# Kernel tuning notes

Measured on AMD Instinct MI355X. Metric: run time of the kernel, lower is better.

Reference implementation:

```python
import jax, jax.numpy as jnp
import numpy as np

NUM_TREES = 32
NUM_NODES = 6
SEED = 0
BATCH, CH, T = 16, 128, 4096


def _make_forest(num_trees, num_nodes, seed):
    """Random rooted trees: node 0 is root, node i>0 attaches to a uniform
    random earlier node (classic random recursive tree). Returns, per tree,
    the children-list representation."""
    rng = np.random.default_rng(seed)
    forest = []
    for _ in range(num_trees):
        children = [[] for _ in range(num_nodes)]
        for i in range(1, num_nodes):
            p = int(rng.integers(0, i))
            children[p].append(i)
        forest.append(children)
    return forest


def _excl_cumsum(u):
    # sum_{s < t} u[..., s]  (exclusive prefix sum along the ordered axis)
    return jnp.cumsum(u, axis=-1) - u


def _sum_trees(x, alphas, forest):
    """Iterated-sums evaluation over a forest in the (plus, times) semiring.
    Node value: v_i(t) = alpha_i * x(t) * prod_{c in children(i)} sum_{s<t} v_c(s).
    Tree output: sum_t v_root(t), per channel. x: [B,C,T]. Returns [B,num_trees,C]."""
    outs = []
    for t_idx, children in enumerate(forest):
        vals = {}
        for i in reversed(range(len(children))):  # leaves-to-root order
            v = alphas[t_idx, i][None, :, None] * x  # [B,C,T]
            for c in children[i]:
                v = v * _excl_cumsum(vals.pop(c))
            vals[i] = v
        outs.append(jnp.sum(vals[0], axis=-1))  # [B,C]
    return jnp.stack(outs, axis=1)  # [B,num_trees,C]


def setup_inputs() -> dict:
    key = jax.random.key(0)
    k1, k2 = jax.random.split(key)
    x = jax.random.normal(k1, (BATCH, CH, T), dtype=jnp.float32)
    alphas = jax.random.normal(k2, (NUM_TREES, NUM_NODES, CH), dtype=jnp.float32)
    return {"x": x, "alphas": alphas}


def reference(x, alphas):
    forest = _make_forest(NUM_TREES, NUM_NODES, SEED)
    return _sum_trees(x, alphas, forest)
```

## Files before the change

kernel.cpp:

```cpp
#include <hip/hip_runtime.h>
#include <cstdint>
#include <cstddef>

namespace cx {

constexpr uint32_t hashmix(uint32_t value, uint32_t& hc) {
    value ^= hc; hc *= 0x931e8875u; value *= hc; value ^= value >> 16; return value;
}
constexpr uint32_t mixf(uint32_t x, uint32_t y) {
    uint32_t r = x * 0xca01f9ddu - y * 0x4973f715u; r ^= r >> 16; return r;
}

struct Pcg64 {
    unsigned __int128 state{}, inc{};
    bool has_uint32{}; uint32_t uinteger{};
    static constexpr unsigned __int128 mult() {
        return (((unsigned __int128)2549297995355413924ULL) << 64) | 4865540595714422341ULL;
    }
    constexpr void step() { state = state * mult() + inc; }
    constexpr void seed_default0() {
        uint32_t pool[4] = {0, 0, 0, 0};
        uint32_t hc = 0x43b0d7e5u;
        for (int i = 0; i < 4; ++i) pool[i] = hashmix(0u, hc);
        for (int isrc = 0; isrc < 4; ++isrc)
            for (int idst = 0; idst < 4; ++idst)
                if (isrc != idst) pool[idst] = mixf(pool[idst], hashmix(pool[isrc], hc));
        uint32_t st[8] = {};
        uint32_t hc2 = 0x8b51f9ddu;
        for (int i = 0; i < 8; ++i) {
            uint32_t dv = pool[i & 3];
            dv ^= hc2; hc2 *= 0x58f38dedu; dv *= hc2; dv ^= dv >> 16;
            st[i] = dv;
        }
        const uint64_t v0 = (uint64_t)st[0] | ((uint64_t)st[1] << 32);
        const uint64_t v1 = (uint64_t)st[2] | ((uint64_t)st[3] << 32);
        const uint64_t v2 = (uint64_t)st[4] | ((uint64_t)st[5] << 32);
        const uint64_t v3 = (uint64_t)st[6] | ((uint64_t)st[7] << 32);
        const unsigned __int128 s = (((unsigned __int128)v0) << 64) | v1;
        const unsigned __int128 i_ = (((unsigned __int128)v2) << 64) | v3;
        state = 0; inc = (i_ << 1) | 1;
        step(); state += s; step();
        has_uint32 = false; uinteger = 0;
    }
    constexpr uint64_t next64() {
        step();
        const uint64_t hi = (uint64_t)(state >> 64), lo = (uint64_t)state;
        const uint64_t x = hi ^ lo;
        const unsigned rot = (unsigned)(state >> 122);
        return (x >> rot) | (x << ((64u - rot) & 63u));
    }
    constexpr uint32_t next32() {
        if (has_uint32) { has_uint32 = false; return uinteger; }
        const uint64_t n = next64();
        has_uint32 = true; uinteger = (uint32_t)(n >> 32);
        return (uint32_t)n;
    }
    constexpr uint32_t bounded_lemire32(uint32_t rng) {
        const uint32_t rng_excl = rng + 1u;
        uint64_t m = (uint64_t)next32() * (uint64_t)rng_excl;
        uint32_t leftover = (uint32_t)m;
        if (leftover < rng_excl) {
            const uint32_t threshold = (0xFFFFFFFFu - rng) % rng_excl;
            while (leftover < threshold) {
                m = (uint64_t)next32() * (uint64_t)rng_excl;
                leftover = (uint32_t)m;
            }
        }
        return (uint32_t)(m >> 32);
    }
    constexpr int64_t integers0(int64_t high) {
        const uint64_t rng = (uint64_t)(high - 1);
        if (rng == 0) return 0;
        return (int64_t)bounded_lemire32((uint32_t)rng);
    }
};

constexpr int NTREE = 32, MAXSER = 32, MAXROOT = 32, MAXFAC = 5, MAXSLOT = 12;

struct Plan {
    int nser, nroot, nslot, maxlvl;
    int lvl[MAXSER];
    int slot[MAXSER];
    int nfac[MAXSER];
    int fac[MAXSER][4];
    int rnfac[MAXROOT];
    int rfac[MAXROOT][MAXFAC];
    int rlvl[MAXROOT];
    int tree_root[NTREE];
};

constexpr Plan build_plan() {
    Plan P{};
    unsigned skey[MAXSER] = {}, rkey[MAXROOT] = {};
    P.nser = 1; skey[0] = (2u << 16) | 2u;
    P.nfac[0] = 0;
    P.nroot = 0;

    Pcg64 rng; rng.seed_default0();
    for (int t = 0; t < NTREE; ++t) {
        int par[6] = {0, 0, 0, 0, 0, 0};
        for (int i = 1; i <= 5; ++i) par[i] = (int)rng.integers0(i);
        int ch[6][5] = {}; int nch[6] = {};
        for (int i = 1; i <= 5; ++i) ch[par[i]][nch[par[i]]++] = i;

        int sid[6] = {}; unsigned keyn[6] = {};
        for (int i = 5; i >= 1; --i) {
            const int n = nch[i];
            unsigned ck[5] = {}; int cf[5] = {};
            for (int k = 0; k < n; ++k) { ck[k] = keyn[ch[i][k]]; cf[k] = sid[ch[i][k]]; }
            for (int a = 0; a < n; ++a)
                for (int bq = a + 1; bq < n; ++bq) {
                    if (ck[bq] > ck[a]) { unsigned tmp = ck[a]; ck[a] = ck[bq]; ck[bq] = tmp; }
                    if (cf[bq] < cf[a]) { int tmp = cf[a]; cf[a] = cf[bq]; cf[bq] = tmp; }
                }
            unsigned bits = 1u, len = 1u;
            for (int k = 0; k < n; ++k) { bits = (bits << (ck[k] >> 16)) | (ck[k] & 0xffffu); len += ck[k] >> 16; }
            bits <<= 1; len += 1;
            const unsigned key = (len << 16) | bits;
            keyn[i] = key;
            int id = -1;
            for (int q = 0; q < P.nser; ++q) if (skey[q] == key) { id = q; break; }
            if (id < 0) {
                id = P.nser++;
                skey[id] = key; P.nfac[id] = n;
                for (int k = 0; k < n; ++k) P.fac[id][k] = cf[k];
            }
            sid[i] = id;
        }
        {
            const int n = nch[0];
            unsigned ck[5] = {}; int cf[5] = {};
            for (int k = 0; k < n; ++k) { ck[k] = keyn[ch[0][k]]; cf[k] = sid[ch[0][k]]; }
            for (int a = 0; a < n; ++a)
                for (int bq = a + 1; bq < n; ++bq) {
                    if (ck[bq] > ck[a]) { unsigned tmp = ck[a]; ck[a] = ck[bq]; ck[bq] = tmp; }
                    if (cf[bq] < cf[a]) { int tmp = cf[a]; cf[a] = cf[bq]; cf[bq] = tmp; }
                }
            unsigned bits = 1u, len = 1u;
            for (int k = 0; k < n; ++k) { bits = (bits << (ck[k] >> 16)) | (ck[k] & 0xffffu); len += ck[k] >> 16; }
            bits <<= 1; len += 1;
            const unsigned key = (len << 16) | bits;
            int id = -1;
            for (int q = 0; q < P.nroot; ++q) if (rkey[q] == key) { id = q; break; }
            if (id < 0) {
                id = P.nroot++;
                rkey[id] = key; P.rnfac[id] = n;
                for (int k = 0; k < n; ++k) P.rfac[id][k] = cf[k];
            }
            P.tree_root[t] = id;
        }
    }
    P.lvl[0] = 0; P.maxlvl = 0;
    for (int s = 1; s < P.nser; ++s) {
        int m = 0;
        for (int k = 0; k < P.nfac[s]; ++k) { const int l = P.lvl[P.fac[s][k]]; if (l > m) m = l; }
        P.lvl[s] = m + 1;
        if (m + 1 > P.maxlvl) P.maxlvl = m + 1;
    }
    for (int r = 0; r < P.nroot; ++r) {
        int m = 0;
        for (int k = 0; k < P.rnfac[r]; ++k) { const int l = P.lvl[P.rfac[r][k]]; if (l > m) m = l; }
        P.rlvl[r] = m;
    }
    int last[MAXSER] = {};
    for (int s = 0; s < P.nser; ++s) last[s] = 0;
    for (int s = 1; s < P.nser; ++s)
        for (int k = 0; k < P.nfac[s]; ++k) { const int f = P.fac[s][k]; if (P.lvl[s] > last[f]) last[f] = P.lvl[s]; }
    for (int r = 0; r < P.nroot; ++r)
        for (int k = 0; k < P.rnfac[r]; ++k) { const int f = P.rfac[r][k]; if (P.rlvl[r] > last[f]) last[f] = P.rlvl[r]; }
    int free_at[MAXSLOT] = {};
    for (int q = 0; q < MAXSLOT; ++q) free_at[q] = -1000;
    P.nslot = 0;
    for (int L = 0; L <= P.maxlvl; ++L)
        for (int s = 0; s < P.nser; ++s) {
            if (P.lvl[s] != L) continue;
            int pick = -1;
            for (int q = 0; q < MAXSLOT; ++q) if (free_at[q] <= L) { pick = q; break; }
            P.slot[s] = pick;
            free_at[pick] = last[s] + 1;
            if (pick + 1 > P.nslot) P.nslot = pick + 1;
        }
    return P;
}

constexpr Plan PL = build_plan();
static_assert(PL.nser <= MAXSER && PL.nroot <= MAXROOT, "plan overflow");
static_assert(PL.nslot <= MAXSLOT && PL.maxlvl <= 9, "plan overflow");
static_assert(PL.nslot >= 1 && PL.nser >= 1 && PL.nroot >= 1, "plan degenerate");

}

template <int CTRL, int RM>
__device__ __forceinline__ float dppmov(float x) {
    return __builtin_bit_cast(float,
        __builtin_amdgcn_update_dpp(0, __builtin_bit_cast(int, x), CTRL, RM, 0xf, false));
}
__device__ __forceinline__ float wave_incl_scan(float v) {
    v += dppmov<0x111, 0xf>(v);
    v += dppmov<0x112, 0xf>(v);
    v += dppmov<0x114, 0xf>(v);
    v += dppmov<0x118, 0xf>(v);
    v += dppmov<0x142, 0xa>(v);
    v += dppmov<0x143, 0xc>(v);
    return v;
}

struct OutMap { unsigned char m[32]; };

__global__ __launch_bounds__(256) void fis_kernel(const float* __restrict__ x,
                                                  const float* __restrict__ alphas,
                                                  float* __restrict__ out,
                                                  const OutMap om) {
    using cx::PL;
    constexpr int NSER = PL.nser, NROOT = PL.nroot, NSLOT = PL.nslot, MAXL = PL.maxlvl;

    const int tid = threadIdx.x;
    const int lane = tid & 63;
    const int wv = tid >> 6;
    const int b = blockIdx.x >> 7;
    const int c = blockIdx.x & 127;

    __shared__ float s_w[NSER + NROOT][4];

    float xr[16];
    {
        const float4* xv = reinterpret_cast<const float4*>(
            x + (((size_t)b << 7) + (size_t)c) * 4096 + (size_t)tid * 16);
#pragma unroll
        for (int j = 0; j < 4; ++j) {
            const float4 v = xv[j];
            xr[4 * j + 0] = v.x; xr[4 * j + 1] = v.y;
            xr[4 * j + 2] = v.z; xr[4 * j + 3] = v.w;
        }
    }

    float S[NSLOT][16];
    float tots[NSER], winc[NSER];

#pragma unroll
    for (int L = 0; L <= MAXL; ++L) {
#pragma unroll
        for (int s = 0; s < NSER; ++s) {
            if (PL.lvl[s] != L) continue;
            constexpr auto& slot = PL.slot;
            const int ds = slot[s];
            float w[16];
#pragma unroll
            for (int j = 0; j < 16; ++j) w[j] = xr[j];
#pragma unroll
            for (int k = 0; k < 4; ++k) {
                if (k < PL.nfac[s]) {
                    const int fs = slot[PL.fac[s][k]];
#pragma unroll
                    for (int j = 0; j < 16; ++j) w[j] *= S[fs][j];
                }
            }
            float run = 0.f;
#pragma unroll
            for (int j = 0; j < 16; ++j) { run += w[j]; S[ds][j] = run; }
            tots[s] = run;
            winc[s] = wave_incl_scan(run);
            if (lane == 63) s_w[s][wv] = winc[s];
        }
        __syncthreads();
#pragma unroll
        for (int s = 0; s < NSER; ++s) {
            if (PL.lvl[s] != L) continue;
            const int ds = PL.slot[s];
            float base = winc[s] - tots[s];
#pragma unroll
            for (int k = 0; k < 3; ++k)
                if (k < wv) base += s_w[s][k];
#pragma unroll
            for (int j = 15; j >= 1; --j) S[ds][j] = base + S[ds][j - 1];
            S[ds][0] = base;
        }
#pragma unroll
        for (int r = 0; r < NROOT; ++r) {
            if (PL.rlvl[r] != L) continue;
            float p[16];
#pragma unroll
            for (int j = 0; j < 16; ++j) p[j] = xr[j];
#pragma unroll
            for (int k = 0; k < 5; ++k) {
                if (k < PL.rnfac[r]) {
                    const int fs = PL.slot[PL.rfac[r][k]];
#pragma unroll
                    for (int j = 0; j < 16; ++j) p[j] *= S[fs][j];
                }
            }
#pragma unroll
            for (int st = 1; st < 16; st <<= 1) {
#pragma unroll
                for (int j = 0; j < 16; j += 2 * st) p[j] += p[j + st];
            }
            const float rt = wave_incl_scan(p[0]);
            if (lane == 63) s_w[NSER + r][wv] = rt;
        }
    }

    __syncthreads();
    if (tid < 32) {
        const int rid = om.m[tid];
        const float T = s_w[NSER + rid][0] + s_w[NSER + rid][1] +
                        s_w[NSER + rid][2] + s_w[NSER + rid][3];
        const float* ap = alphas + tid * 768 + c;
        const float aprod = ap[0] * ap[128] * ap[256] * ap[384] * ap[512] * ap[640];
        out[(((size_t)b << 5) + (size_t)tid) * 128 + c] = aprod * T;
    }
}

extern "C" void kernel_launch(void* const* d_in, const int* in_sizes, int n_in,
                              void* d_out, int out_size, void* d_ws, size_t ws_size,
                              hipStream_t stream) {
    const float* x = (const float*)d_in[0];
    const float* alphas = (const float*)d_in[1];
    float* out = (float*)d_out;

    OutMap om;
    for (int t = 0; t < cx::NTREE; ++t) om.m[t] = (unsigned char)cx::PL.tree_root[t];

    fis_kernel<<<dim3(16 * 128), dim3(256), 0, stream>>>(x, alphas, out, om);
}
```

Measured before the change: 19.79 us.

## Use 512-thread blocks with 8 elements per thread and fused exclusive scans

Doubles threads per block to 512 and halves the per-thread chunk of the time axis to 8 elements. This cuts per-thread register arrays so more waves can be resident, and it adds a launch-bounds occupancy hint. The serial scan now builds the exclusive prefix directly, folding the last child factor into an FMA instead of shifting the array afterwards. The root reduction becomes an FMA dot product. In exchange, the cross-wave combine now spans 8 waves, adding shared-memory reads and synchronisation cost per level.

```diff
diff --git a/kernel.cpp b/kernel.cpp
--- a/kernel.cpp
+++ b/kernel.cpp
@@ -207,10 +207,14 @@
 
 struct OutMap { unsigned char m[32]; };
 
-__global__ __launch_bounds__(256) void fis_kernel(const float* __restrict__ x,
-                                                  const float* __restrict__ alphas,
-                                                  float* __restrict__ out,
-                                                  const OutMap om) {
+#define THREADS 512
+#define ELEM 8
+#define NWAVE 8
+
+__global__ __launch_bounds__(THREADS, 6) void fis_kernel(const float* __restrict__ x,
+                                                         const float* __restrict__ alphas,
+                                                         float* __restrict__ out,
+                                                         const OutMap om) {
     using cx::PL;
     constexpr int NSER = PL.nser, NROOT = PL.nroot, NSLOT = PL.nslot, MAXL = PL.maxlvl;
 
@@ -220,90 +224,94 @@
     const int b = blockIdx.x >> 7;
     const int c = blockIdx.x & 127;
 
-    __shared__ float s_w[NSER + NROOT][4];
-
-    float xr[16];
+    __shared__ float s_w[NSER + NROOT][NWAVE];
+
+    float xr[ELEM];
     {
         const float4* xv = reinterpret_cast<const float4*>(
-            x + (((size_t)b << 7) + (size_t)c) * 4096 + (size_t)tid * 16);
-#pragma unroll
-        for (int j = 0; j < 4; ++j) {
-            const float4 v = xv[j];
-            xr[4 * j + 0] = v.x; xr[4 * j + 1] = v.y;
-            xr[4 * j + 2] = v.z; xr[4 * j + 3] = v.w;
-        }
-    }
-
-    float S[NSLOT][16];
-    float tots[NSER], winc[NSER];
+            x + (((size_t)b << 7) + (size_t)c) * 4096 + (size_t)tid * ELEM);
+        const float4 v0 = xv[0], v1 = xv[1];
+        xr[0] = v0.x; xr[1] = v0.y; xr[2] = v0.z; xr[3] = v0.w;
+        xr[4] = v1.x; xr[5] = v1.y; xr[6] = v1.z; xr[7] = v1.w;
+    }
+
+    float S[NSLOT][ELEM];
+    float wex[cx::MAXSER];
 
 #pragma unroll
     for (int L = 0; L <= MAXL; ++L) {
-#pragma unroll
-        for (int s = 0; s < NSER; ++s) {
-            if (PL.lvl[s] != L) continue;
-            constexpr auto& slot = PL.slot;
-            const int ds = slot[s];
-            float w[16];
-#pragma unroll
-            for (int j = 0; j < 16; ++j) w[j] = xr[j];
-#pragma unroll
-            for (int k = 0; k < 4; ++k) {
-                if (k < PL.nfac[s]) {
-                    const int fs = slot[PL.fac[s][k]];
-#pragma unroll
-                    for (int j = 0; j < 16; ++j) w[j] *= S[fs][j];
-                }
-            }
-            float run = 0.f;
-#pragma unroll
-            for (int j = 0; j < 16; ++j) { run += w[j]; S[ds][j] = run; }
-            tots[s] = run;
-            winc[s] = wave_incl_scan(run);
-            if (lane == 63) s_w[s][wv] = winc[s];
-        }
-        __syncthreads();
 #pragma unroll
         for (int s = 0; s < NSER; ++s) {
             if (PL.lvl[s] != L) continue;
             const int ds = PL.slot[s];
-            float base = winc[s] - tots[s];
-#pragma unroll
-            for (int k = 0; k < 3; ++k)
+            float run = 0.f;
+            if (PL.nfac[s] == 0) {
+#pragma unroll
+                for (int j = 0; j < ELEM; ++j) { S[ds][j] = run; run += xr[j]; }
+            } else {
+                float v[ELEM];
+#pragma unroll
+                for (int j = 0; j < ELEM; ++j) v[j] = xr[j];
+#pragma unroll
+                for (int k = 0; k < 3; ++k) {
+                    if (k < PL.nfac[s] - 1) {
+                        const int fs = PL.slot[PL.fac[s][k]];
+#pragma unroll
+                        for (int j = 0; j < ELEM; ++j) v[j] *= S[fs][j];
+                    }
+                }
+                const int fl = PL.slot[PL.fac[s][PL.nfac[s] - 1]];
+#pragma unroll
+                for (int j = 0; j < ELEM; ++j) {
+                    S[ds][j] = run;
+                    run = __builtin_fmaf(v[j], S[fl][j], run);
+                }
+            }
+            const float wi = wave_incl_scan(run);
+            if (lane == 63) s_w[s][wv] = wi;
+            wex[s] = wi - run;
+        }
+        __syncthreads();
+#pragma unroll
+        for (int s = 0; s < NSER; ++s) {
+            if (PL.lvl[s] != L) continue;
+            const int ds = PL.slot[s];
+            float base = wex[s];
+#pragma unroll
+            for (int k = 0; k < NWAVE - 1; ++k)
                 if (k < wv) base += s_w[s][k];
 #pragma unroll
-            for (int j = 15; j >= 1; --j) S[ds][j] = base + S[ds][j - 1];
-            S[ds][0] = base;
+            for (int j = 0; j < ELEM; ++j) S[ds][j] += base;
         }
 #pragma unroll
         for (int r = 0; r < NROOT; ++r) {
             if (PL.rlvl[r] != L) continue;
-            float p[16];
-#pragma unroll
-            for (int j = 0; j < 16; ++j) p[j] = xr[j];
-#pragma unroll
-            for (int k = 0; k < 5; ++k) {
-                if (k < PL.rnfac[r]) {
+            float v[ELEM];
+#pragma unroll
+            for (int j = 0; j < ELEM; ++j) v[j] = xr[j];
+#pragma unroll
+            for (int k = 0; k < 4; ++k) {
+                if (k < PL.rnfac[r] - 1) {
                     const int fs = PL.slot[PL.rfac[r][k]];
 #pragma unroll
-                    for (int j = 0; j < 16; ++j) p[j] *= S[fs][j];
-                }
-            }
-#pragma unroll
-            for (int st = 1; st < 16; st <<= 1) {
-#pragma unroll
-                for (int j = 0; j < 16; j += 2 * st) p[j] += p[j + st];
-            }
-            const float rt = wave_incl_scan(p[0]);
-            if (lane == 63) s_w[NSER + r][wv] = rt;
+                    for (int j = 0; j < ELEM; ++j) v[j] *= S[fs][j];
+                }
+            }
+            const int fl = PL.slot[PL.rfac[r][PL.rnfac[r] - 1]];
+            float acc = 0.f;
+#pragma unroll
+            for (int j = 0; j < ELEM; ++j) acc = __builtin_fmaf(v[j], S[fl][j], acc);
+            const float wr = wave_incl_scan(acc);
+            if (lane == 63) s_w[NSER + r][wv] = wr;
         }
     }
 
     __syncthreads();
     if (tid < 32) {
         const int rid = om.m[tid];
-        const float T = s_w[NSER + rid][0] + s_w[NSER + rid][1] +
-                        s_w[NSER + rid][2] + s_w[NSER + rid][3];
+        float T = 0.f;
+#pragma unroll
+        for (int k = 0; k < NWAVE; ++k) T += s_w[NSER + rid][k];
         const float* ap = alphas + tid * 768 + c;
         const float aprod = ap[0] * ap[128] * ap[256] * ap[384] * ap[512] * ap[640];
         out[(((size_t)b << 5) + (size_t)tid) * 128 + c] = aprod * T;
@@ -320,5 +328,5 @@
     OutMap om;
     for (int t = 0; t < cx::NTREE; ++t) om.m[t] = (unsigned char)cx::PL.tree_root[t];
 
-    fis_kernel<<<dim3(16 * 128), dim3(256), 0, stream>>>(x, alphas, out, om);
-}
+    fis_kernel<<<dim3(16 * 128), dim3(THREADS), 0, stream>>>(x, alphas, out, om);
+}
```

Result: slower. 64.59 us (+226.4%).
